# Kernel optimization log

Measured on AMD Instinct MI355X. Metric: run time of the kernel, lower is better.

## Reference

```python
import jax, jax.numpy as jnp
import numpy as np

N_HEAD = 16

def setup_inputs() -> dict:
    key = jax.random.key(0)
    ks = jax.random.split(key, 4)
    B, S, E = 2, 2048, 1024
    x = jax.random.normal(ks[0], (B, S, E), dtype=jnp.float32)
    W_qkv = jax.random.normal(ks[1], (E, 3 * E), dtype=jnp.float32) * (1.0 / np.sqrt(E))
    b_qkv = jnp.zeros((3 * E,), dtype=jnp.float32)
    W_proj = jax.random.normal(ks[2], (E, E), dtype=jnp.float32) * (1.0 / np.sqrt(E))
    b_proj = jnp.zeros((E,), dtype=jnp.float32)
    return {"x": x, "W_qkv": W_qkv, "b_qkv": b_qkv, "W_proj": W_proj, "b_proj": b_proj}


def reference(x, W_qkv, b_qkv, W_proj, b_proj):
    B, S, E = x.shape
    H = N_HEAD
    D = E // H
    scale = 1.0 / np.sqrt(D).astype(np.float32)

    qkv = x @ W_qkv + b_qkv                      # [B,S,3E]
    q, k, v = jnp.split(qkv, 3, axis=2)
    # Original code does .view(B, H, S, D) directly (no transpose); replicate exactly.
    q = q.reshape(B, H, S, D)
    k = k.reshape(B, H, S, D)
    v = v.reshape(B, H, S, D)

    att = jnp.einsum('bhqd,bhkd->bhqk', q, k) * scale   # [B,H,S,S]
    causal = jnp.tril(jnp.ones((S, S), dtype=bool))      # True = visible
    att = jnp.where(causal[None, None], att, jnp.float32(-jnp.inf))
    att = jax.nn.softmax(att, axis=-1)
    # dropout is identity in eval mode (p used only at train)
    res = jnp.einsum('bhqk,bhkd->bhqd', att, v)           # [B,H,S,D]
    res = res.transpose(0, 2, 1, 3).reshape(B, S, E)      # matches transpose(1,2).view
    return res @ W_proj + b_proj
```

## Files before the change

kernel.cpp:

```cpp
#include <hip/hip_runtime.h>
#include <hip/hip_bf16.h>

using bf16 = __hip_bfloat16;
using s16x8 = __attribute__((ext_vector_type(8))) short;
using f32x4 = __attribute__((ext_vector_type(4))) float;
using f32x16 = __attribute__((ext_vector_type(16))) float;
typedef unsigned short u16;
typedef unsigned int u32;

#define DEVINL __device__ __forceinline__

DEVINL u16 f2bf(float f) {
  u32 u = __float_as_uint(f);
  u32 r = (u + 0x7fffu + ((u >> 16) & 1u)) >> 16;
  return (u16)r;
}

DEVINL u32 pkbf(float a, float b) {
  __hip_bfloat162 h = __float22bfloat162_rn(make_float2(a, b));
  union { __hip_bfloat162 h; u32 u; } c;
  c.h = h;
  return c.u;
}

DEVINL void gload_lds16(const void* g, void* l) {
  __builtin_amdgcn_global_load_lds(
      (__attribute__((address_space(1))) void*)(void*)(g),
      (__attribute__((address_space(3))) void*)(l), 16, 0, 0);
}

__global__ __launch_bounds__(256) void cast_f32_bf16(
    const float* __restrict__ in, bf16* __restrict__ out, int n) {
  int i = (blockIdx.x * 256 + threadIdx.x) * 8;
  float4 a = *(const float4*)(in + i);
  float4 b = *(const float4*)(in + i + 4);
  u16 tmp[8] = {f2bf(a.x), f2bf(a.y), f2bf(a.z), f2bf(a.w),
                f2bf(b.x), f2bf(b.y), f2bf(b.z), f2bf(b.w)};
  *(uint4*)(out + i) = *(const uint4*)tmp;
}

__global__ __launch_bounds__(256) void transpose_cast(
    const float* __restrict__ W, bf16* __restrict__ Wt, int K, int N) {
  __shared__ float tile[64][65];
  int n0 = blockIdx.x * 64, k0 = blockIdx.y * 64;
  int t = threadIdx.x;
#pragma unroll
  for (int i = 0; i < 16; ++i) {
    int idx = i * 256 + t;
    int r = idx >> 6, c = idx & 63;
    tile[r][c] = W[(size_t)(k0 + r) * N + n0 + c];
  }
  __syncthreads();
#pragma unroll
  for (int i = 0; i < 16; ++i) {
    int idx = i * 256 + t;
    int r = idx >> 6, c = idx & 63;
    Wt[(size_t)(n0 + r) * K + k0 + c] = __float2bfloat16(tile[c][r]);
  }
}

__global__ __launch_bounds__(256) void v_transpose(
    const bf16* __restrict__ vb, bf16* __restrict__ vt) {
  __shared__ u16 lt[64][68];
  const int bh = blockIdx.y;
  const int s0 = blockIdx.x * 64;
  const int tid = threadIdx.x;
  const bf16* src = vb + (size_t)bh * 131072;
#pragma unroll
  for (int i = 0; i < 2; ++i) {
    int c = i * 256 + tid;
    int srow = c >> 3, sc = (c & 7) * 8;
    uint4 v = *(const uint4*)(src + (size_t)(s0 + srow) * 64 + sc);
    const u16* e = (const u16*)&v;
#pragma unroll
    for (int j = 0; j < 8; ++j) lt[srow][sc + j] = e[j];
  }
  __syncthreads();
#pragma unroll
  for (int i = 0; i < 2; ++i) {
    int c = i * 256 + tid;
    int drow = c >> 3, sc = (c & 7) * 8;
    u16 tmp[8];
#pragma unroll
    for (int j = 0; j < 8; ++j) tmp[j] = lt[sc + j][drow];
    *(uint4*)(vt + (size_t)(bh * 64 + drow) * 2048 + s0 + sc) = *(const uint4*)tmp;
  }
}

template <int MODE>
__global__ __launch_bounds__(256) void gemm_bt(
    const bf16* __restrict__ A, const bf16* __restrict__ Bt,
    const float* __restrict__ bias,
    bf16* __restrict__ q, bf16* __restrict__ k, bf16* __restrict__ v,
    float* __restrict__ outf, int M, int N, int K) {
  __shared__ bf16 As[128 * 64];
  __shared__ bf16 Bs[128 * 64];
  const int tid = threadIdx.x;
  const int w = tid >> 6, lane = tid & 63;
  const int lr = lane >> 4, lc = lane & 15;
  const int wr = w >> 1, wc = w & 1;
  const int m0 = blockIdx.x * 128, n0 = blockIdx.y * 128;

  f32x4 acc[4][4] = {};

  const int srow = lane >> 3;
  const int scolb = ((lane & 7) * 16) ^ (srow << 4);
  const char* Abase = (const char*)(A + (size_t)m0 * K);
  const char* Bbase = (const char*)(Bt + (size_t)n0 * K);
  const int Krow = K * 2;

  for (int kt = 0; kt < K; kt += 64) {
    __syncthreads();
#pragma unroll
    for (int c = 0; c < 4; ++c) {
      int row = w * 32 + c * 8 + srow;
      gload_lds16(Abase + (size_t)row * Krow + kt * 2 + scolb,
                  (char*)As + w * 4096 + c * 1024 + lane * 16);
    }
#pragma unroll
    for (int c = 0; c < 4; ++c) {
      int row = w * 32 + c * 8 + srow;
      gload_lds16(Bbase + (size_t)row * Krow + kt * 2 + scolb,
                  (char*)Bs + w * 4096 + c * 1024 + lane * 16);
    }
    __syncthreads();
#pragma unroll
    for (int ks = 0; ks < 2; ++ks) {
      s16x8 af[4], bfr[4];
#pragma unroll
      for (int mi = 0; mi < 4; ++mi) {
        int row = wr * 64 + mi * 16 + lc;
        int colb = (ks * 64 + lr * 16) ^ ((row & 7) << 4);
        af[mi] = *(const s16x8*)((const char*)As + row * 128 + colb);
      }
#pragma unroll
      for (int ni = 0; ni < 4; ++ni) {
        int row = wc * 64 + ni * 16 + lc;
        int colb = (ks * 64 + lr * 16) ^ ((row & 7) << 4);
        bfr[ni] = *(const s16x8*)((const char*)Bs + row * 128 + colb);
      }
#pragma unroll
      for (int mi = 0; mi < 4; ++mi)
#pragma unroll
        for (int ni = 0; ni < 4; ++ni)
          acc[mi][ni] = __builtin_amdgcn_mfma_f32_16x16x32_bf16(
              af[mi], bfr[ni], acc[mi][ni], 0, 0, 0);
    }
  }

#pragma unroll
  for (int mi = 0; mi < 4; ++mi) {
#pragma unroll
    for (int ni = 0; ni < 4; ++ni) {
      int col = n0 + wc * 64 + ni * 16 + lc;
      float bb = bias[col];
      int rowb = m0 + wr * 64 + mi * 16 + lr * 4;
#pragma unroll
      for (int r = 0; r < 4; ++r) {
        float val = acc[mi][ni][r] + bb;
        int row = rowb + r;
        if (MODE == 0) {
          if (col < 1024) val *= 0.125f;
          bf16* o = (col < 1024) ? q : ((col < 2048) ? k : v);
          int cc = col & 1023;
          o[(size_t)row * 1024 + cc] = __float2bfloat16(val);
        } else {
          outf[(size_t)row * N + col] = val;
        }
      }
    }
  }
}

__global__ __launch_bounds__(256) void attn_kernel(
    const bf16* __restrict__ qb, const bf16* __restrict__ kb,
    const bf16* __restrict__ vtp, bf16* __restrict__ ob) {
  const int idx = blockIdx.x;
  const int bh_lo = idx & 7;
  const int r0 = idx >> 3;
  const int bh = ((r0 >> 4) << 3) + bh_lo;
  const int qbk = 15 - (r0 & 15);
  const int b = bh >> 4, h = bh & 15;
  const int tid = threadIdx.x;
  const int w = tid >> 6;
  const int lane = tid & 63;
  const int l31 = lane & 31;
  const int hi = lane >> 5;

  const int jj = qbk * 4 + w;
  const int qbase = jj * 32;
  const int qg = qbase + l31;

  const size_t hb = (size_t)bh * 131072;
  const bf16* qh = qb + hb;
  const bf16* kh = kb + hb;
  const bf16* vh = vtp + hb;

  s16x8 qf[4];
#pragma unroll
  for (int db = 0; db < 4; ++db)
    qf[db] = *(const s16x8*)(qh + (size_t)(qbase + l31) * 64 + db * 16 + hi * 8);

  f32x16 o0 = {}, o1 = {};
  float m_run = -INFINITY, l_run = 0.f;
  const float LOG2E = 1.44269504f;

  const int nt = (qbase >> 6) + 1;
  for (int t = 0; t < nt; ++t) {
    f32x16 s0 = {}, s1 = {};
#pragma unroll
    for (int db = 0; db < 4; ++db) {
      s16x8 kf0 = *(const s16x8*)(kh + (size_t)(t * 64 + l31) * 64 + db * 16 + hi * 8);
      s0 = __builtin_amdgcn_mfma_f32_32x32x16_bf16(kf0, qf[db], s0, 0, 0, 0);
    }
#pragma unroll
    for (int db = 0; db < 4; ++db) {
      s16x8 kf1 = *(const s16x8*)(kh + (size_t)(t * 64 + 32 + l31) * 64 + db * 16 + hi * 8);
      s1 = __builtin_amdgcn_mfma_f32_32x32x16_bf16(kf1, qf[db], s1, 0, 0, 0);
    }

    if (t == nt - 1) {
#pragma unroll
      for (int r = 0; r < 16; ++r) {
        int kvr = t * 64 + (r & 3) + 8 * (r >> 2) + 4 * hi;
        if (kvr > qg) s0[r] = -INFINITY;
        if (kvr + 32 > qg) s1[r] = -INFINITY;
      }
    }

    float mx[16];
#pragma unroll
    for (int r = 0; r < 16; ++r) mx[r] = fmaxf(s0[r], s1[r]);
#pragma unroll
    for (int off = 8; off >= 1; off >>= 1)
#pragma unroll
      for (int r = 0; r < 8; ++r)
        if (r < off) mx[r] = fmaxf(mx[r], mx[r + off]);
    float mxv = fmaxf(mx[0], __shfl_xor(mx[0], 32));

    if (!__all(mxv <= m_run + 8.f)) {
      float mnew = fmaxf(m_run, mxv);
      float sf = exp2f((m_run - mnew) * LOG2E);
      m_run = mnew;
      l_run *= sf;
#pragma unroll
      for (int r = 0; r < 16; ++r) {
        float sfr = __shfl(sf, (r & 3) + 8 * (r >> 2) + 4 * hi);
        o0[r] *= sfr;
        o1[r] *= sfr;
      }
    }

    const float nmC = -m_run * LOG2E;
    float ps[16];
#pragma unroll
    for (int r = 0; r < 16; ++r) {
      float p0 = exp2f(__builtin_fmaf(s0[r], LOG2E, nmC));
      float p1 = exp2f(__builtin_fmaf(s1[r], LOG2E, nmC));
      s0[r] = p0;
      s1[r] = p1;
      ps[r] = p0 + p1;
    }
#pragma unroll
    for (int off = 8; off >= 1; off >>= 1)
#pragma unroll
      for (int r = 0; r < 8; ++r)
        if (r < off) ps[r] += ps[r + off];
    l_run += ps[0] + __shfl_xor(ps[0], 32);

    s16x8 vf[4][2];
#pragma unroll
    for (int cc = 0; cc < 4; ++cc)
#pragma unroll
      for (int ds = 0; ds < 2; ++ds)
        vf[cc][ds] = *(const s16x8*)(vh + (size_t)(ds * 32 + l31) * 2048 +
                                     t * 64 + cc * 16 + hi * 8);

    auto mk = [&](float p0, float p1, float p2, float p3,
                  float p4, float p5, float p6, float p7) -> s16x8 {
      u32 A0 = pkbf(p0, p1), A1 = pkbf(p2, p3);
      u32 C0 = pkbf(p4, p5), C1 = pkbf(p6, p7);
      u32 pA0 = (u32)__shfl_xor((int)A0, 32);
      u32 pA1 = (u32)__shfl_xor((int)A1, 32);
      u32 pC0 = (u32)__shfl_xor((int)C0, 32);
      u32 pC1 = (u32)__shfl_xor((int)C1, 32);
      union { u32 u[4]; s16x8 v; } f;
      f.u[0] = hi ? pC0 : A0;
      f.u[1] = hi ? pC1 : A1;
      f.u[2] = hi ? C0 : pA0;
      f.u[3] = hi ? C1 : pA1;
      return f.v;
    };
    s16x8 pa[4];
    pa[0] = mk(s0[0], s0[1], s0[2], s0[3], s0[4], s0[5], s0[6], s0[7]);
    pa[1] = mk(s0[8], s0[9], s0[10], s0[11], s0[12], s0[13], s0[14], s0[15]);
    pa[2] = mk(s1[0], s1[1], s1[2], s1[3], s1[4], s1[5], s1[6], s1[7]);
    pa[3] = mk(s1[8], s1[9], s1[10], s1[11], s1[12], s1[13], s1[14], s1[15]);

#pragma unroll
    for (int cc = 0; cc < 4; ++cc) {
      o0 = __builtin_amdgcn_mfma_f32_32x32x16_bf16(pa[cc], vf[cc][0], o0, 0, 0, 0);
      o1 = __builtin_amdgcn_mfma_f32_32x32x16_bf16(pa[cc], vf[cc][1], o1, 0, 0, 0);
    }
  }

  float inv = 1.f / l_run;
#pragma unroll
  for (int r = 0; r < 16; ++r) {
    int qrow = (r & 3) + 8 * (r >> 2) + 4 * hi;
    float ivr = __shfl(inv, qrow);
    bf16* orow = ob + (size_t)(b * 2048 + qbase + qrow) * 1024 + h * 64;
    orow[l31] = __float2bfloat16(o0[r] * ivr);
    orow[32 + l31] = __float2bfloat16(o1[r] * ivr);
  }
}

extern "C" void kernel_launch(void* const* d_in, const int* in_sizes, int n_in,
                              void* d_out, int out_size, void* d_ws, size_t ws_size,
                              hipStream_t stream) {
  const float* x = (const float*)d_in[0];
  const float* Wqkv = (const float*)d_in[1];
  const float* bqkv = (const float*)d_in[2];
  const float* Wproj = (const float*)d_in[3];
  const float* bproj = (const float*)d_in[4];
  float* out = (float*)d_out;

  char* ws = (char*)d_ws;
  bf16* xb = (bf16*)(ws);
  bf16* Wt1 = (bf16*)(ws + 8388608);
  bf16* Wt2 = (bf16*)(ws + 14680064);
  bf16* qb = (bf16*)(ws + 16777216);
  bf16* kb = (bf16*)(ws + 25165824);
  bf16* vb = (bf16*)(ws + 33554432);
  bf16* vtb = (bf16*)(ws + 41943040);
  bf16* Ob = xb;

  cast_f32_bf16<<<2048, 256, 0, stream>>>(x, xb, 4096 * 1024);
  transpose_cast<<<dim3(48, 16), 256, 0, stream>>>(Wqkv, Wt1, 1024, 3072);
  transpose_cast<<<dim3(16, 16), 256, 0, stream>>>(Wproj, Wt2, 1024, 1024);
  gemm_bt<0><<<dim3(32, 24), 256, 0, stream>>>(xb, Wt1, bqkv, qb, kb, vb, nullptr,
                                               4096, 3072, 1024);
  v_transpose<<<dim3(32, 32), 256, 0, stream>>>(vb, vtb);
  attn_kernel<<<512, 256, 0, stream>>>(qb, kb, vtb, Ob);
  gemm_bt<1><<<dim3(32, 8), 256, 0, stream>>>(Ob, Wt2, bproj, nullptr, nullptr, nullptr,
                                              out, 4096, 1024, 1024);
}
```

Before: 289.2 us.

## Stage K/V tiles in swizzled LDS with double-buffered async loads in attention

The attention kernel now cooperatively loads each 64-row K and V^T tile into shared memory with direct global-to-LDS loads, double-buffered so the next tile is fetched while the current one is computed. An XOR swizzle on the LDS layout is meant to avoid bank conflicts on the MFMA fragment reads. This replaces per-wave redundant global reads of the same K/V tiles with one shared copy per block. In exchange it adds a block-wide barrier every iteration, and waves whose causal range ends early sit idle until the block's last wave finishes its tiles.

```diff
diff --git a/kernel.cpp b/kernel.cpp
--- a/kernel.cpp
+++ b/kernel.cpp
@@ -175,6 +175,9 @@
 __global__ __launch_bounds__(256) void attn_kernel(
     const bf16* __restrict__ qb, const bf16* __restrict__ kb,
     const bf16* __restrict__ vtp, bf16* __restrict__ ob) {
+  __shared__ bf16 Kl[2][64 * 64];
+  __shared__ bf16 Vl[2][64 * 64];
+
   const int idx = blockIdx.x;
   const int bh_lo = idx & 7;
   const int r0 = idx >> 3;
@@ -193,8 +196,11 @@
 
   const size_t hb = (size_t)bh * 131072;
   const bf16* qh = qb + hb;
-  const bf16* kh = kb + hb;
-  const bf16* vh = vtp + hb;
+  const char* khc = (const char*)(kb + hb);
+  const char* vhc = (const char*)(vtp + hb);
+
+  const int srow = lane >> 3;
+  const int scolb = ((lane & 7) * 16) ^ (srow << 4);
 
   s16x8 qf[4];
 #pragma unroll
@@ -205,103 +211,136 @@
   float m_run = -INFINITY, l_run = 0.f;
   const float LOG2E = 1.44269504f;
 
-  const int nt = (qbase >> 6) + 1;
-  for (int t = 0; t < nt; ++t) {
-    f32x16 s0 = {}, s1 = {};
-#pragma unroll
-    for (int db = 0; db < 4; ++db) {
-      s16x8 kf0 = *(const s16x8*)(kh + (size_t)(t * 64 + l31) * 64 + db * 16 + hi * 8);
-      s0 = __builtin_amdgcn_mfma_f32_32x32x16_bf16(kf0, qf[db], s0, 0, 0, 0);
-    }
-#pragma unroll
-    for (int db = 0; db < 4; ++db) {
-      s16x8 kf1 = *(const s16x8*)(kh + (size_t)(t * 64 + 32 + l31) * 64 + db * 16 + hi * 8);
-      s1 = __builtin_amdgcn_mfma_f32_32x32x16_bf16(kf1, qf[db], s1, 0, 0, 0);
-    }
-
-    if (t == nt - 1) {
+  const int nt_w = (qbase >> 6) + 1;
+  const int NT = 2 * qbk + 2;
+
+  auto STAGE = [&](int bf, int t) {
+#pragma unroll
+    for (int c = 0; c < 2; ++c) {
+      int lrow = w * 16 + c * 8 + srow;
+      gload_lds16(khc + (size_t)(t * 64 + lrow) * 128 + scolb,
+                  (char*)Kl[bf] + (w * 16 + c * 8) * 128 + lane * 16);
+      gload_lds16(vhc + (size_t)lrow * 4096 + (size_t)t * 128 + scolb,
+                  (char*)Vl[bf] + (w * 16 + c * 8) * 128 + lane * 16);
+    }
+  };
+
+  STAGE(0, 0);
+  __syncthreads();
+
+  int cur = 0;
+  for (int t = 0; t < NT; ++t) {
+    if (t + 1 < NT) STAGE(cur ^ 1, t + 1);
+
+    if (t < nt_w) {
+      const char* Kb = (const char*)Kl[cur];
+      const char* Vb = (const char*)Vl[cur];
+
+      f32x16 s0 = {}, s1 = {};
+#pragma unroll
+      for (int db = 0; db < 4; ++db) {
+        int row = l31;
+        s16x8 kf0 = *(const s16x8*)(Kb + row * 128 +
+                                    ((db * 32 + hi * 16) ^ ((row & 7) << 4)));
+        s0 = __builtin_amdgcn_mfma_f32_32x32x16_bf16(kf0, qf[db], s0, 0, 0, 0);
+      }
+#pragma unroll
+      for (int db = 0; db < 4; ++db) {
+        int row = 32 + l31;
+        s16x8 kf1 = *(const s16x8*)(Kb + row * 128 +
+                                    ((db * 32 + hi * 16) ^ ((row & 7) << 4)));
+        s1 = __builtin_amdgcn_mfma_f32_32x32x16_bf16(kf1, qf[db], s1, 0, 0, 0);
+      }
+
+      if (t == nt_w - 1) {
+#pragma unroll
+        for (int r = 0; r < 16; ++r) {
+          int kvr = t * 64 + (r & 3) + 8 * (r >> 2) + 4 * hi;
+          if (kvr > qg) s0[r] = -INFINITY;
+          if (kvr + 32 > qg) s1[r] = -INFINITY;
+        }
+      }
+
+      float mx[16];
+#pragma unroll
+      for (int r = 0; r < 16; ++r) mx[r] = fmaxf(s0[r], s1[r]);
+#pragma unroll
+      for (int off = 8; off >= 1; off >>= 1)
+#pragma unroll
+        for (int r = 0; r < 8; ++r)
+          if (r < off) mx[r] = fmaxf(mx[r], mx[r + off]);
+      float mxv = fmaxf(mx[0], __shfl_xor(mx[0], 32));
+
+      if (!__all(mxv <= m_run + 8.f)) {
+        float mnew = fmaxf(m_run, mxv);
+        float sf = exp2f((m_run - mnew) * LOG2E);
+        m_run = mnew;
+        l_run *= sf;
+#pragma unroll
+        for (int r = 0; r < 16; ++r) {
+          float sfr = __shfl(sf, (r & 3) + 8 * (r >> 2) + 4 * hi);
+          o0[r] *= sfr;
+          o1[r] *= sfr;
+        }
+      }
+
+      const float nmC = -m_run * LOG2E;
+      float ps[16];
 #pragma unroll
       for (int r = 0; r < 16; ++r) {
-        int kvr = t * 64 + (r & 3) + 8 * (r >> 2) + 4 * hi;
-        if (kvr > qg) s0[r] = -INFINITY;
-        if (kvr + 32 > qg) s1[r] = -INFINITY;
-      }
-    }
-
-    float mx[16];
-#pragma unroll
-    for (int r = 0; r < 16; ++r) mx[r] = fmaxf(s0[r], s1[r]);
-#pragma unroll
-    for (int off = 8; off >= 1; off >>= 1)
-#pragma unroll
-      for (int r = 0; r < 8; ++r)
-        if (r < off) mx[r] = fmaxf(mx[r], mx[r + off]);
-    float mxv = fmaxf(mx[0], __shfl_xor(mx[0], 32));
-
-    if (!__all(mxv <= m_run + 8.f)) {
-      float mnew = fmaxf(m_run, mxv);
-      float sf = exp2f((m_run - mnew) * LOG2E);
-      m_run = mnew;
-      l_run *= sf;
-#pragma unroll
-      for (int r = 0; r < 16; ++r) {
-        float sfr = __shfl(sf, (r & 3) + 8 * (r >> 2) + 4 * hi);
-        o0[r] *= sfr;
-        o1[r] *= sfr;
-      }
-    }
-
-    const float nmC = -m_run * LOG2E;
-    float ps[16];
-#pragma unroll
-    for (int r = 0; r < 16; ++r) {
-      float p0 = exp2f(__builtin_fmaf(s0[r], LOG2E, nmC));
-      float p1 = exp2f(__builtin_fmaf(s1[r], LOG2E, nmC));
-      s0[r] = p0;
-      s1[r] = p1;
-      ps[r] = p0 + p1;
-    }
-#pragma unroll
-    for (int off = 8; off >= 1; off >>= 1)
-#pragma unroll
-      for (int r = 0; r < 8; ++r)
-        if (r < off) ps[r] += ps[r + off];
-    l_run += ps[0] + __shfl_xor(ps[0], 32);
-
-    s16x8 vf[4][2];
-#pragma unroll
-    for (int cc = 0; cc < 4; ++cc)
-#pragma unroll
-      for (int ds = 0; ds < 2; ++ds)
-        vf[cc][ds] = *(const s16x8*)(vh + (size_t)(ds * 32 + l31) * 2048 +
-                                     t * 64 + cc * 16 + hi * 8);
-
-    auto mk = [&](float p0, float p1, float p2, float p3,
-                  float p4, float p5, float p6, float p7) -> s16x8 {
-      u32 A0 = pkbf(p0, p1), A1 = pkbf(p2, p3);
-      u32 C0 = pkbf(p4, p5), C1 = pkbf(p6, p7);
-      u32 pA0 = (u32)__shfl_xor((int)A0, 32);
-      u32 pA1 = (u32)__shfl_xor((int)A1, 32);
-      u32 pC0 = (u32)__shfl_xor((int)C0, 32);
-      u32 pC1 = (u32)__shfl_xor((int)C1, 32);
-      union { u32 u[4]; s16x8 v; } f;
-      f.u[0] = hi ? pC0 : A0;
-      f.u[1] = hi ? pC1 : A1;
-      f.u[2] = hi ? C0 : pA0;
-      f.u[3] = hi ? C1 : pA1;
-      return f.v;
-    };
-    s16x8 pa[4];
-    pa[0] = mk(s0[0], s0[1], s0[2], s0[3], s0[4], s0[5], s0[6], s0[7]);
-    pa[1] = mk(s0[8], s0[9], s0[10], s0[11], s0[12], s0[13], s0[14], s0[15]);
-    pa[2] = mk(s1[0], s1[1], s1[2], s1[3], s1[4], s1[5], s1[6], s1[7]);
-    pa[3] = mk(s1[8], s1[9], s1[10], s1[11], s1[12], s1[13], s1[14], s1[15]);
-
-#pragma unroll
-    for (int cc = 0; cc < 4; ++cc) {
-      o0 = __builtin_amdgcn_mfma_f32_32x32x16_bf16(pa[cc], vf[cc][0], o0, 0, 0, 0);
-      o1 = __builtin_amdgcn_mfma_f32_32x32x16_bf16(pa[cc], vf[cc][1], o1, 0, 0, 0);
-    }
+        float p0 = exp2f(__builtin_fmaf(s0[r], LOG2E, nmC));
+        float p1 = exp2f(__builtin_fmaf(s1[r], LOG2E, nmC));
+        s0[r] = p0;
+        s1[r] = p1;
+        ps[r] = p0 + p1;
+      }
+#pragma unroll
+      for (int off = 8; off >= 1; off >>= 1)
+#pragma unroll
+        for (int r = 0; r < 8; ++r)
+          if (r < off) ps[r] += ps[r + off];
+      l_run += ps[0] + __shfl_xor(ps[0], 32);
+
+      s16x8 vf[4][2];
+#pragma unroll
+      for (int cc = 0; cc < 4; ++cc)
+#pragma unroll
+        for (int ds = 0; ds < 2; ++ds) {
+          int row = ds * 32 + l31;
+          vf[cc][ds] = *(const s16x8*)(Vb + row * 128 +
+                                       ((cc * 32 + hi * 16) ^ ((row & 7) << 4)));
+        }
+
+      auto mk = [&](float p0, float p1, float p2, float p3,
+                    float p4, float p5, float p6, float p7) -> s16x8 {
+        u32 A0 = pkbf(p0, p1), A1 = pkbf(p2, p3);
+        u32 C0 = pkbf(p4, p5), C1 = pkbf(p6, p7);
+        u32 pA0 = (u32)__shfl_xor((int)A0, 32);
+        u32 pA1 = (u32)__shfl_xor((int)A1, 32);
+        u32 pC0 = (u32)__shfl_xor((int)C0, 32);
+        u32 pC1 = (u32)__shfl_xor((int)C1, 32);
+        union { u32 u[4]; s16x8 v; } f;
+        f.u[0] = hi ? pC0 : A0;
+        f.u[1] = hi ? pC1 : A1;
+        f.u[2] = hi ? C0 : pA0;
+        f.u[3] = hi ? C1 : pA1;
+        return f.v;
+      };
+      s16x8 pa[4];
+      pa[0] = mk(s0[0], s0[1], s0[2], s0[3], s0[4], s0[5], s0[6], s0[7]);
+      pa[1] = mk(s0[8], s0[9], s0[10], s0[11], s0[12], s0[13], s0[14], s0[15]);
+      pa[2] = mk(s1[0], s1[1], s1[2], s1[3], s1[4], s1[5], s1[6], s1[7]);
+      pa[3] = mk(s1[8], s1[9], s1[10], s1[11], s1[12], s1[13], s1[14], s1[15]);
+
+#pragma unroll
+      for (int cc = 0; cc < 4; ++cc) {
+        o0 = __builtin_amdgcn_mfma_f32_32x32x16_bf16(pa[cc], vf[cc][0], o0, 0, 0, 0);
+        o1 = __builtin_amdgcn_mfma_f32_32x32x16_bf16(pa[cc], vf[cc][1], o1, 0, 0, 0);
+      }
+    }
+
+    __syncthreads();
+    cur ^= 1;
   }
 
   float inv = 1.f / l_run;
```

After: 238.6 us. -17.5%, faster.
